# Performance work log

Measured on AMD Instinct MI355X. Metric: run time of the kernel, lower is better.

Reference implementation:

```python
import jax, jax.numpy as jnp
import numpy as np

B, N, C_IN = 8, 16384, 64
NPOINTS = 1024     # S: number of sampled centers (FPS)
NNEI = 32          # K: neighbors per center (ball query cap)
RADIUS = 0.2
EPS = 1e-5


def fps(pos, S):
    """Farthest point sampling, deterministic start at index 0. pos: [B,N,3] -> [B,S] int32."""
    b, n, _ = pos.shape

    def step(carry, _):
        dist, far = carry
        centroid = jnp.take_along_axis(pos, far[:, None, None], axis=1)  # [B,1,3]
        d = jnp.sum((pos - centroid) ** 2, axis=-1)                       # [B,N]
        dist = jnp.minimum(dist, d)
        return (dist, jnp.argmax(dist, axis=-1).astype(jnp.int32)), far

    init = (jnp.full((b, n), 1e10, pos.dtype), jnp.zeros((b,), jnp.int32))
    _, cent = jax.lax.scan(step, init, None, length=S)  # [S,B]
    return cent.T                                        # [B,S]


def gather(points, idx):
    """points [B,N,C], idx [B,...] -> [B,...,C] (per-batch fancy gather)."""
    return jax.vmap(lambda p, i: p[i])(points, idx)


def ball_query(pos, centers, radius, k):
    """Fixed-radius neighbor search. pos [B,N,3], centers [B,S,3] -> idx [B,S,K] int32.
    Pads short neighborhoods with the first in-radius point (the center itself)."""
    n = pos.shape[1]
    sqr = jnp.sum((centers[:, :, None, :] - pos[:, None, :, :]) ** 2, axis=-1)  # [B,S,N]
    idx = jnp.where(sqr <= radius * radius, jnp.arange(n, dtype=jnp.int32), n)
    idx = jnp.sort(idx, axis=-1)[..., :k]                                        # [B,S,K]
    first = idx[..., :1]
    return jnp.where(idx == n, first, idx)


def conv_bn_relu(x, w, b, g, be):
    """1x1 Conv2d + BatchNorm2d(training stats) + ReLU over grouped tensor x [B,S,K,Cin]."""
    h = jnp.einsum('bskc,cd->bskd', x, w) + b
    mu = jnp.mean(h, axis=(0, 1, 2), keepdims=True)
    var = jnp.mean((h - mu) ** 2, axis=(0, 1, 2), keepdims=True)
    h = (h - mu) * jax.lax.rsqrt(var + EPS) * g + be
    return jax.nn.relu(h)


def reference(pos, feat,
              w_sem1, b_sem1, g_sem1, be_sem1, w_sem2, b_sem2, g_sem2, be_sem2,
              w_geo1, b_geo1, g_geo1, be_geo1, w_geo2, b_geo2, g_geo2, be_geo2):
    centroids = fps(pos, NPOINTS)                       # [B,S]
    centers = gather(pos, centroids)                    # [B,S,3]
    idx = ball_query(pos, centers, RADIUS, NNEI)        # [B,S,K]

    grouped_pos = gather(pos, idx)                      # [B,S,K,3]
    grouped_feat = gather(feat, idx)                    # [B,S,K,C]
    center_rep = jnp.broadcast_to(centers[:, :, None, :], grouped_pos.shape)
    geo_in = jnp.concatenate([center_rep, grouped_pos], axis=-1)  # [B,S,K,6]

    h = conv_bn_relu(grouped_feat, w_sem1, b_sem1, g_sem1, be_sem1)
    h = conv_bn_relu(h, w_sem2, b_sem2, g_sem2, be_sem2)
    h_sem = jnp.max(h, axis=2)                          # [B,S,Cout] max-pool over neighbors

    hg = conv_bn_relu(geo_in, w_geo1, b_geo1, g_geo1, be_geo1)
    hg = conv_bn_relu(hg, w_geo2, b_geo2, g_geo2, be_geo2)
    h_geo = jnp.max(hg, axis=2)                         # [B,S,Cout]

    # original concatenates semantic and geo node features along dim 0
    return jnp.concatenate([h_sem, h_geo], axis=0)      # [2B,S,Cout]


def setup_inputs() -> dict:
    key = jax.random.key(0)
    ks = jax.random.split(key, 12)
    d = {
        'pos': jax.random.uniform(ks[0], (B, N, 3), jnp.float32),
        'feat': jax.random.normal(ks[1], (B, N, C_IN), jnp.float32),
        'w_sem1': jax.random.normal(ks[2], (64, 64), jnp.float32) * 0.05,
        'b_sem1': jnp.zeros((64,), jnp.float32),
        'g_sem1': jnp.ones((64,), jnp.float32),
        'be_sem1': jnp.zeros((64,), jnp.float32),
        'w_sem2': jax.random.normal(ks[3], (64, 128), jnp.float32) * 0.05,
        'b_sem2': jnp.zeros((128,), jnp.float32),
        'g_sem2': jnp.ones((128,), jnp.float32),
        'be_sem2': jnp.zeros((128,), jnp.float32),
        'w_geo1': jax.random.normal(ks[4], (6, 64), jnp.float32) * 0.05,
        'b_geo1': jnp.zeros((64,), jnp.float32),
        'g_geo1': jnp.ones((64,), jnp.float32),
        'be_geo1': jnp.zeros((64,), jnp.float32),
        'w_geo2': jax.random.normal(ks[5], (64, 128), jnp.float32) * 0.05,
        'b_geo2': jnp.zeros((128,), jnp.float32),
        'g_geo2': jnp.ones((128,), jnp.float32),
        'be_geo2': jnp.zeros((128,), jnp.float32),
    }
    return d
```

## Files before the change

kernel.cpp:

```cpp
#include <hip/hip_runtime.h>

#define NB 8
#define NPTS 16384
#define S 1024
#define KNEI 32
#define MROWS (NB*S*KNEI)

typedef float v2f __attribute__((ext_vector_type(2)));

#define DPP_MAXF0(CTRL, v) do {                                               \
    int _o = __builtin_amdgcn_update_dpp(0, __float_as_int(v),                \
                                         (CTRL), 0xF, 0xF, true);             \
    (v) = fmaxf((v), __int_as_float(_o));                                     \
  } while (0)

#define DPP_MINI(CTRL, v) do {                                                \
    int _o = __builtin_amdgcn_update_dpp((int)0x7fffffff, (v),                \
                                         (CTRL), 0xF, 0xF, false);            \
    (v) = (_o < (v)) ? _o : (v);                                              \
  } while (0)

#define DPP_MAXK0(CTRL, k) do {                                               \
    int _olo = __builtin_amdgcn_update_dpp(0, (int)(unsigned)(k),             \
                                           (CTRL), 0xF, 0xF, true);           \
    int _ohi = __builtin_amdgcn_update_dpp(0, (int)(unsigned)((k) >> 32),     \
                                           (CTRL), 0xF, 0xF, true);           \
    unsigned long long _ok = (((unsigned long long)(unsigned)_ohi) << 32)     \
                           | (unsigned)_olo;                                  \
    if (_ok > (k)) (k) = _ok;                                                 \
  } while (0)

#define DPP_ROW_SHR1   0x111
#define DPP_ROW_SHR2   0x112
#define DPP_ROW_SHR4   0x114
#define DPP_ROW_SHR8   0x118
#define DPP_ROW_BCAST15 0x142
#define DPP_ROW_BCAST31 0x143

__global__ __launch_bounds__(1024, 4) void fps_kernel(const float* __restrict__ pos,
                                                      float* __restrict__ centers,
                                                      float* __restrict__ sbuf){
#pragma clang fp contract(off)
  __shared__ int hist[4096];
  __shared__ int ts[1024];
  __shared__ unsigned short perm[16384];
  __shared__ unsigned long long lslotK[2][16];
  const int b = blockIdx.x;
  const int t = threadIdx.x;
  const int wid = t >> 6, lane = t & 63;
  const float* pb = pos + (size_t)b * NPTS * 3;
  float* ssx = sbuf + (size_t)b * 3 * NPTS;
  float* ssy = ssx + NPTS;
  float* ssz = ssy + NPTS;
  const int p0 = t * 16;

  float c[48];
  {
    const float4* src = (const float4*)(pb + (size_t)t*48);
#pragma unroll
    for (int q = 0; q < 12; ++q) *(float4*)&c[q*4] = src[q];
  }
  int cell[16];
#pragma unroll
  for (int j = 0; j < 16; ++j){
    float x = c[3*j], y = c[3*j+1], z = c[3*j+2];
    int ix = (int)(x * 16.f); ix = ix < 0 ? 0 : (ix > 15 ? 15 : ix);
    int iy = (int)(y * 16.f); iy = iy < 0 ? 0 : (iy > 15 ? 15 : iy);
    int iz = (int)(z * 16.f); iz = iz < 0 ? 0 : (iz > 15 ? 15 : iz);
    int m = 0;
#pragma unroll
    for (int k = 0; k < 4; ++k){
      m |= ((ix >> k) & 1) << (3*k + 2);
      m |= ((iy >> k) & 1) << (3*k + 1);
      m |= ((iz >> k) & 1) << (3*k + 0);
    }
    cell[j] = m;
  }
#pragma unroll
  for (int i = 0; i < 4; ++i) hist[t*4 + i] = 0;
  __syncthreads();
#pragma unroll
  for (int j = 0; j < 16; ++j) atomicAdd(&hist[cell[j]], 1);
  __syncthreads();
  int h0 = hist[t*4], h1 = hist[t*4+1], h2v = hist[t*4+2];
  ts[t] = h0 + h1 + h2v + hist[t*4+3];
  __syncthreads();
  for (int off = 1; off < 1024; off <<= 1){
    int add = (t >= off) ? ts[t - off] : 0;
    __syncthreads();
    ts[t] += add;
    __syncthreads();
  }
  {
    int base = (t == 0) ? 0 : ts[t-1];
    hist[t*4]   = base;
    hist[t*4+1] = base + h0;
    hist[t*4+2] = base + h0 + h1;
    hist[t*4+3] = base + h0 + h1 + h2v;
  }
  __syncthreads();
#pragma unroll
  for (int j = 0; j < 16; ++j){
    int dst = atomicAdd(&hist[cell[j]], 1);
    ssx[dst] = c[3*j];
    ssy[dst] = c[3*j+1];
    ssz[dst] = c[3*j+2];
    perm[dst] = (unsigned short)(p0 + j);
  }
  __syncthreads();

  v2f px[8], py[8], pz[8], dist[8];
  int perm_reg[8];
#pragma unroll
  for (int g = 0; g < 4; ++g){
    float4 vx = *(const float4*)&ssx[p0 + g*4];
    float4 vy = *(const float4*)&ssy[p0 + g*4];
    float4 vz = *(const float4*)&ssz[p0 + g*4];
    px[g*2]   = (v2f){vx.x, vx.y}; px[g*2+1] = (v2f){vx.z, vx.w};
    py[g*2]   = (v2f){vy.x, vy.y}; py[g*2+1] = (v2f){vy.z, vy.w};
    pz[g*2]   = (v2f){vz.x, vz.y}; pz[g*2+1] = (v2f){vz.z, vz.w};
  }
#pragma unroll
  for (int j = 0; j < 8; ++j){
    perm_reg[j] = (int)perm[p0 + 2*j] | ((int)perm[p0 + 2*j + 1] << 16);
  }
  float bxl = 1e30f, bxh = -1e30f, byl = 1e30f, byh = -1e30f;
  float bzl = 1e30f, bzh = -1e30f;
#pragma unroll
  for (int j = 0; j < 8; ++j){
    asm volatile("" : "+v"(px[j]), "+v"(py[j]), "+v"(pz[j]), "+v"(perm_reg[j]));
    bxl = fminf(bxl, fminf(px[j].x, px[j].y));
    bxh = fmaxf(bxh, fmaxf(px[j].x, px[j].y));
    byl = fminf(byl, fminf(py[j].x, py[j].y));
    byh = fmaxf(byh, fmaxf(py[j].x, py[j].y));
    bzl = fminf(bzl, fminf(pz[j].x, pz[j].y));
    bzh = fmaxf(bzh, fmaxf(pz[j].x, pz[j].y));
    dist[j] = (v2f){1e10f, 1e10f};
  }
  float ub = 1e10f;
  unsigned long long key = 0;
  float cx = pb[0], cy = pb[1], cz = pb[2];

  for (int s = 0; s < S; ++s){
    if (t == 0){
      float* cd = centers + (size_t)(b*S + s)*3;
      cd[0] = cx; cd[1] = cy; cd[2] = cz;
    }
    float lx = fmaxf(fmaxf(bxl - cx, cx - bxh), 0.f);
    float ly = fmaxf(fmaxf(byl - cy, cy - byh), 0.f);
    float lz = fmaxf(fmaxf(bzl - cz, cz - bzh), 0.f);
    float lb2 = ((lx*lx + ly*ly) + lz*lz);
    bool act = !(lb2 * 0.99999f >= ub);
    unsigned long long am = __ballot((int)act);
    if (am){
      if (act){
        v2f cx2 = (v2f){cx, cx}, cy2 = (v2f){cy, cy}, cz2 = (v2f){cz, cz};
        float nb = 0.0f;
#pragma unroll
        for (int j = 0; j < 8; ++j){
          v2f dx = px[j] - cx2;
          v2f dy = py[j] - cy2;
          v2f dz = pz[j] - cz2;
          v2f t1 = dx * dx;
          v2f t2 = dy * dy;
          v2f t3 = dz * dz;
          v2f d  = (t1 + t2) + t3;
          v2f od = dist[j];
          v2f nd = (v2f){__builtin_fminf(od.x, d.x), __builtin_fminf(od.y, d.y)};
          dist[j] = nd;
          nb = fmaxf(fmaxf(nb, nd.x), nd.y);
        }
        ub = nb;
      }
      float bv = ub;
      DPP_MAXF0(DPP_ROW_SHR1,   bv);
      DPP_MAXF0(DPP_ROW_SHR2,   bv);
      DPP_MAXF0(DPP_ROW_SHR4,   bv);
      DPP_MAXF0(DPP_ROW_SHR8,   bv);
      DPP_MAXF0(DPP_ROW_BCAST15, bv);
      DPP_MAXF0(DPP_ROW_BCAST31, bv);
      float bmw = __int_as_float(
          __builtin_amdgcn_readlane(__float_as_int(bv), 63));
      int mi = 0x7fffffff;
      if (ub == bmw){
#pragma unroll
        for (int j = 0; j < 8; ++j){
          if (dist[j].x == bmw){ int o = perm_reg[j] & 0xffff;         mi = o < mi ? o : mi; }
          if (dist[j].y == bmw){ int o = (perm_reg[j] >> 16) & 0xffff; mi = o < mi ? o : mi; }
        }
      }
      DPP_MINI(DPP_ROW_SHR1,   mi);
      DPP_MINI(DPP_ROW_SHR2,   mi);
      DPP_MINI(DPP_ROW_SHR4,   mi);
      DPP_MINI(DPP_ROW_SHR8,   mi);
      DPP_MINI(DPP_ROW_BCAST15, mi);
      DPP_MINI(DPP_ROW_BCAST31, mi);
      int miw = __builtin_amdgcn_readlane(mi, 63);
      key = ((unsigned long long)__float_as_uint(bmw) << 15)
          | (unsigned long long)(16384 - miw);
    }
    const int par = s & 1;
    if (lane == 0) lslotK[par][wid] = key;
    __syncthreads();
    unsigned long long kk = lslotK[par][lane & 15];
    int ufi_l = 16384 - (int)(kk & 0x7FFFull);
    const float* cpl = pb + (size_t)ufi_l*3;
    float wx = cpl[0], wy = cpl[1], wz = cpl[2];
    unsigned long long kko = kk;
    DPP_MAXK0(DPP_ROW_SHR1, kk);
    DPP_MAXK0(DPP_ROW_SHR2, kk);
    DPP_MAXK0(DPP_ROW_SHR4, kk);
    DPP_MAXK0(DPP_ROW_SHR8, kk);
    unsigned blo = (unsigned)__builtin_amdgcn_readlane((int)(unsigned)kk, 15);
    unsigned bhi = (unsigned)__builtin_amdgcn_readlane((int)(unsigned)(kk >> 32), 15);
    unsigned long long bkmax = (((unsigned long long)bhi) << 32) | blo;
    unsigned m16 = (unsigned)__ballot((int)(kko == bkmax)) & 0xffffu;
    int sidx = (int)__builtin_ctz(m16);
    cx = __int_as_float(__builtin_amdgcn_readlane(__float_as_int(wx), sidx));
    cy = __int_as_float(__builtin_amdgcn_readlane(__float_as_int(wy), sidx));
    cz = __int_as_float(__builtin_amdgcn_readlane(__float_as_int(wz), sidx));
  }
}

__global__ __launch_bounds__(256) void ballq_kernel(const float* __restrict__ pos,
                                                    const float* __restrict__ centers,
                                                    int* __restrict__ idx,
                                                    float* __restrict__ stats){
#pragma clang fp contract(off)
  if (blockIdx.x < 3) stats[blockIdx.x*256 + threadIdx.x] = 0.f;
  const float R2 = (float)(0.2*0.2);
  int wid  = blockIdx.x*4 + (threadIdx.x >> 6);
  int lane = threadIdx.x & 63;
  int b = wid >> 10;
  const float* pb = pos + (size_t)b * NPTS * 3;
  float cx = centers[wid*3+0], cy = centers[wid*3+1], cz = centers[wid*3+2];
  int* out = idx + wid*KNEI;
  int count = 0; int first = -1;
  for (int base = 0; base < NPTS; base += 64){
    int p = base + lane;
    float dx = pb[p*3+0]-cx, dy = pb[p*3+1]-cy, dz = pb[p*3+2]-cz;
    float t1 = dx*dx, t2 = dy*dy, t3 = dz*dz;
    float d = (t1 + t2) + t3;
    bool inr = d <= R2;
    unsigned long long mask = __ballot(inr);
    if (count == 0 && mask) first = base + __builtin_ctzll(mask);
    if (inr){
      int slot = count + __popcll(mask & ((1ull << lane) - 1ull));
      if (slot < KNEI) out[slot] = p;
    }
    count += __popcll(mask);
    if (count >= KNEI) break;
  }
  if (count < KNEI){
    for (int slot = count + lane; slot < KNEI; slot += 64) out[slot] = first;
  }
}

__global__ __launch_bounds__(256) void gemm1_both(const float* __restrict__ feat,
    const float* __restrict__ pos, const float* __restrict__ centers,
    const int* __restrict__ idx,
    const float* __restrict__ w_s, const float* __restrict__ b_s,
    float* __restrict__ h1s, float* __restrict__ st_s,
    const float* __restrict__ w_g, const float* __restrict__ b_g,
    float* __restrict__ h1g, float* __restrict__ st_g){
  __shared__ float smem[8448];
  const int tid = threadIdx.x;
  if (blockIdx.x < (MROWS/64)){
    float (*xst)[66] = (float(*)[66])smem;
    float (*wsh)[64] = (float(*)[64])(smem + 4224);
    const int m0 = blockIdx.x * 64;
#pragma unroll
    for (int i = 0; i < 4; ++i){
      int q = tid + i*256;
      int r = q >> 4, c4 = q & 15;
      *(float4*)&wsh[r][c4*4] = *(const float4*)&w_s[r*64 + c4*4];
    }
#pragma unroll
    for (int i = 0; i < 4; ++i){
      int q = tid + i*256;
      int r = q >> 4, c4 = q & 15;
      int m = m0 + r;
      int nb = idx[m];
      int b = m >> 15;
      const float* fr = feat + ((size_t)b*NPTS + nb)*64;
      float4 v = *(const float4*)&fr[c4*4];
      xst[c4*4+0][r] = v.x;
      xst[c4*4+1][r] = v.y;
      xst[c4*4+2][r] = v.z;
      xst[c4*4+3][r] = v.w;
    }
    __syncthreads();
    const int g  = tid & 7;
    const int rt = tid >> 3;
    const int r0 = rt * 2;
    float acc[2][8];
#pragma unroll
    for (int c = 0; c < 8; ++c){ float bb = b_s[g*8+c]; acc[0][c] = bb; acc[1][c] = bb; }
    for (int k = 0; k < 64; ++k){
      float x0 = xst[k][r0], x1 = xst[k][r0+1];
      float4 wa = *(float4*)&wsh[k][g*8];
      float4 wb = *(float4*)&wsh[k][g*8+4];
      float wv[8] = {wa.x,wa.y,wa.z,wa.w,wb.x,wb.y,wb.z,wb.w};
#pragma unroll
      for (int c = 0; c < 8; ++c){ acc[0][c] += x0*wv[c]; acc[1][c] += x1*wv[c]; }
    }
#pragma unroll
    for (int r = 0; r < 2; ++r){
      float* dst = h1s + (size_t)(m0 + r0 + r)*64 + g*8;
      *(float4*)dst     = make_float4(acc[r][0],acc[r][1],acc[r][2],acc[r][3]);
      *(float4*)(dst+4) = make_float4(acc[r][4],acc[r][5],acc[r][6],acc[r][7]);
    }
    float ls[8], lq[8];
#pragma unroll
    for (int c = 0; c < 8; ++c){
      ls[c] = acc[0][c] + acc[1][c];
      lq[c] = acc[0][c]*acc[0][c] + acc[1][c]*acc[1][c];
    }
    __syncthreads();
    float* red  = smem;
    float* redq = smem + 4224;
#pragma unroll
    for (int c = 0; c < 8; ++c){
      red[(g*8+c)*32 + rt]  = ls[c];
      redq[(g*8+c)*32 + rt] = lq[c];
    }
    __syncthreads();
    if (tid < 128){
      int c = tid & 63;
      const float* src = (tid < 64) ? red : redq;
      float a2 = 0.f;
      for (int i = 0; i < 32; ++i) a2 += src[c*32+i];
      atomicAdd(&st_s[(tid < 64 ? 0 : 64) + c], a2);
    }
  } else {
    float (*xs)[8]   = (float(*)[8])smem;
    float (*wsh)[64] = (float(*)[64])(smem + 512);
    float* red  = smem + 896;
    float* redq = smem + 2944;
    const int m0 = (blockIdx.x - (MROWS/64)) * 64;
    for (int i = tid; i < 384; i += 256) wsh[i >> 6][i & 63] = w_g[i];
    if (tid < 64){
      int m = m0 + tid;
      int grp = m >> 5;
      int b = m >> 15;
      int nb = idx[m];
      const float* cp = centers + (size_t)grp*3;
      const float* pp = pos + ((size_t)b*NPTS + nb)*3;
      xs[tid][0]=cp[0]; xs[tid][1]=cp[1]; xs[tid][2]=cp[2];
      xs[tid][3]=pp[0]; xs[tid][4]=pp[1]; xs[tid][5]=pp[2];
    }
    __syncthreads();
    const int g  = tid & 7;
    const int rt = tid >> 3;
    const int r0 = rt * 2;
    float acc[2][8];
#pragma unroll
    for (int c = 0; c < 8; ++c){ float bb = b_g[g*8+c]; acc[0][c]=bb; acc[1][c]=bb; }
#pragma unroll
    for (int k = 0; k < 6; ++k){
      float x0 = xs[r0][k], x1 = xs[r0+1][k];
      float4 wa = *(float4*)&wsh[k][g*8];
      float4 wb = *(float4*)&wsh[k][g*8+4];
      float wv[8] = {wa.x,wa.y,wa.z,wa.w,wb.x,wb.y,wb.z,wb.w};
#pragma unroll
      for (int c = 0; c < 8; ++c){ acc[0][c] += x0*wv[c]; acc[1][c] += x1*wv[c]; }
    }
#pragma unroll
    for (int r = 0; r < 2; ++r){
      float* dst = h1g + (size_t)(m0 + r0 + r)*64 + g*8;
      *(float4*)dst     = make_float4(acc[r][0],acc[r][1],acc[r][2],acc[r][3]);
      *(float4*)(dst+4) = make_float4(acc[r][4],acc[r][5],acc[r][6],acc[r][7]);
    }
    float ls[8], lq[8];
#pragma unroll
    for (int c = 0; c < 8; ++c){
      ls[c] = acc[0][c] + acc[1][c];
      lq[c] = acc[0][c]*acc[0][c] + acc[1][c]*acc[1][c];
    }
#pragma unroll
    for (int c = 0; c < 8; ++c){
      red[(g*8+c)*32 + rt]  = ls[c];
      redq[(g*8+c)*32 + rt] = lq[c];
    }
    __syncthreads();
    if (tid < 128){
      int c = tid & 63;
      const float* src = (tid < 64) ? red : redq;
      float a2 = 0.f;
      for (int i = 0; i < 32; ++i) a2 += src[c*32+i];
      atomicAdd(&st_g[(tid < 64 ? 0 : 64) + c], a2);
    }
  }
}

__global__ __launch_bounds__(256) void gemm2_both(
    const float* __restrict__ h1s, const float* __restrict__ st1,
    const float* __restrict__ g1,  const float* __restrict__ be1,
    const float* __restrict__ w_s2, const float* __restrict__ b_s2,
    float* __restrict__ hmax1, float* __restrict__ st2,
    const float* __restrict__ h1g, const float* __restrict__ st3,
    const float* __restrict__ g3,  const float* __restrict__ be3,
    const float* __restrict__ w_g2, const float* __restrict__ b_g2,
    float* __restrict__ hmax2, float* __restrict__ st4){
  __shared__ float smem[12416];
  __shared__ float abuf[64], dbuf[64];
  const int tid = threadIdx.x;
  const bool sem = blockIdx.x < (MROWS/64);
  const int bx = sem ? blockIdx.x : blockIdx.x - (MROWS/64);
  const float* hin  = sem ? h1s  : h1g;
  const float* w    = sem ? w_s2 : w_g2;
  const float* bias = sem ? b_s2 : b_g2;
  float* hmax       = sem ? hmax1 : hmax2;
  float* stat       = sem ? st2  : st4;
  float (*xst)[66]  = (float(*)[66])smem;
  float (*wsh)[128] = (float(*)[128])(smem + 4224);
  const int m0 = bx * 64;
  if (tid < 64){
    const float* st  = sem ? st1 : st3;
    const float* gam = sem ? g1  : g3;
    const float* bet = sem ? be1 : be3;
    const float invM = 1.0f / (float)MROWS;
    float mu  = st[tid] * invM;
    float ex2 = st[64 + tid] * invM;
    float var = ex2 - mu*mu;
    float aa = gam[tid] * rsqrtf(var + 1e-5f);
    abuf[tid] = aa;
    dbuf[tid] = bet[tid] - mu*aa;
  }
  __syncthreads();
#pragma unroll
  for (int i = 0; i < 8; ++i){
    int q = tid + i*256;
    int r = q >> 5, c4 = q & 31;
    *(float4*)&wsh[r][c4*4] = *(const float4*)&w[r*128 + c4*4];
  }
#pragma unroll
  for (int i = 0; i < 4; ++i){
    int q = tid + i*256;
    int r = q >> 4, c4 = q & 15;
    float4 v = *(const float4*)&hin[(size_t)(m0+r)*64 + c4*4];
    float a0 = abuf[c4*4+0], aA = abuf[c4*4+1], aB = abuf[c4*4+2], aC = abuf[c4*4+3];
    float d0 = dbuf[c4*4+0], dA = dbuf[c4*4+1], dB = dbuf[c4*4+2], dC = dbuf[c4*4+3];
    v.x = fmaxf(v.x*a0 + d0, 0.f);
    v.y = fmaxf(v.y*aA + dA, 0.f);
    v.z = fmaxf(v.z*aB + dB, 0.f);
    v.w = fmaxf(v.w*aC + dC, 0.f);
    xst[c4*4+0][r] = v.x;
    xst[c4*4+1][r] = v.y;
    xst[c4*4+2][r] = v.z;
    xst[c4*4+3][r] = v.w;
  }
  __syncthreads();
  const int g  = tid & 15;
  const int rt = tid >> 4;
  const int r0 = rt * 4;
  float acc[4][8];
#pragma unroll
  for (int c = 0; c < 8; ++c){
    float bb = bias[g*8+c];
    acc[0][c]=bb; acc[1][c]=bb; acc[2][c]=bb; acc[3][c]=bb;
  }
  for (int k = 0; k < 64; ++k){
    float x0 = xst[k][r0], x1 = xst[k][r0+1], x2 = xst[k][r0+2], x3 = xst[k][r0+3];
    float4 wa = *(float4*)&wsh[k][g*8];
    float4 wb = *(float4*)&wsh[k][g*8+4];
    float wv[8] = {wa.x,wa.y,wa.z,wa.w,wb.x,wb.y,wb.z,wb.w};
#pragma unroll
    for (int c = 0; c < 8; ++c){
      acc[0][c] += x0*wv[c]; acc[1][c] += x1*wv[c];
      acc[2][c] += x2*wv[c]; acc[3][c] += x3*wv[c];
    }
  }
  float ls[8], lq[8], tmax[8];
#pragma unroll
  for (int c = 0; c < 8; ++c){
    ls[c] = acc[0][c]+acc[1][c]+acc[2][c]+acc[3][c];
    lq[c] = acc[0][c]*acc[0][c]+acc[1][c]*acc[1][c]+acc[2][c]*acc[2][c]+acc[3][c]*acc[3][c];
    tmax[c] = fmaxf(fmaxf(acc[0][c],acc[1][c]), fmaxf(acc[2][c],acc[3][c]));
  }
  __syncthreads();
  float* red  = smem;
  float* mred = smem + 4224;
#pragma unroll
  for (int c = 0; c < 8; ++c){
    red[(g*8+c)*16 + rt]        = ls[c];
    red[2048 + (g*8+c)*16 + rt] = lq[c];
    mred[rt*128 + g*8 + c]      = tmax[c];
  }
  __syncthreads();
  {
    int c = tid & 127;
    int isq = tid >> 7;
    float a2 = 0.f;
    for (int i = 0; i < 16; ++i) a2 += red[isq*2048 + c*16 + i];
    atomicAdd(&stat[isq*128 + c], a2);
  }
  {
    int og = tid >> 7;
    int c  = tid & 127;
    float m = -3.4e38f;
#pragma unroll
    for (int i = 0; i < 8; ++i) m = fmaxf(m, mred[(og*8 + i)*128 + c]);
    hmax[(size_t)(bx*2 + og)*128 + c] = m;
  }
}

__global__ __launch_bounds__(256) void bnapply_both(const float* __restrict__ hmax1,
    const float* __restrict__ st2, const float* __restrict__ g2,
    const float* __restrict__ be2,
    const float* __restrict__ hmax2,
    const float* __restrict__ st4, const float* __restrict__ g4,
    const float* __restrict__ be4,
    float* __restrict__ out){
  const int half = NB*S*128;
  int i = blockIdx.x*256 + threadIdx.x;
  bool semh = i < half;
  int j = semh ? i : i - half;
  int c = j & 127;
  const float* st  = semh ? st2 : st4;
  const float* gam = semh ? g2  : g4;
  const float* bet = semh ? be2 : be4;
  const float invM = 1.0f / (float)MROWS;
  float mu  = st[c] * invM;
  float ex2 = st[128 + c] * invM;
  float var = ex2 - mu*mu;
  float aa = gam[c] * rsqrtf(var + 1e-5f);
  float dd = bet[c] - mu*aa;
  float hv = semh ? hmax1[j] : hmax2[j];
  out[i] = fmaxf(hv*aa + dd, 0.f);
}

extern "C" void kernel_launch(void* const* d_in, const int* in_sizes, int n_in,
                              void* d_out, int out_size, void* d_ws, size_t ws_size,
                              hipStream_t stream){
  const float* pos   = (const float*)d_in[0];
  const float* feat  = (const float*)d_in[1];
  const float* w_s1  = (const float*)d_in[2];
  const float* b_s1  = (const float*)d_in[3];
  const float* g_s1  = (const float*)d_in[4];
  const float* be_s1 = (const float*)d_in[5];
  const float* w_s2  = (const float*)d_in[6];
  const float* b_s2  = (const float*)d_in[7];
  const float* g_s2  = (const float*)d_in[8];
  const float* be_s2 = (const float*)d_in[9];
  const float* w_g1  = (const float*)d_in[10];
  const float* b_g1  = (const float*)d_in[11];
  const float* g_g1  = (const float*)d_in[12];
  const float* be_g1 = (const float*)d_in[13];
  const float* w_g2  = (const float*)d_in[14];
  const float* b_g2  = (const float*)d_in[15];
  const float* g_g2  = (const float*)d_in[16];
  const float* be_g2 = (const float*)d_in[17];
  float* outp = (float*)d_out;
  float* wsf  = (float*)d_ws;

  float* centers = wsf;
  int*   idxp    = (int*)(wsf + 24576);
  float* stats   = wsf + 24576 + 262144;
  float* h1s     = wsf + 288256;
  float* h1g     = h1s + (size_t)MROWS*64;
  float* sortbuf = h1g + (size_t)MROWS*64;
  float* hmax1   = sortbuf + 393216;
  float* hmax2   = hmax1 + 1048576;

  float* st1 = stats;
  float* st2 = stats + 128;
  float* st3 = stats + 384;
  float* st4 = stats + 512;

  fps_kernel<<<NB, 1024, 0, stream>>>(pos, centers, sortbuf);
  ballq_kernel<<<(NB*S)/4, 256, 0, stream>>>(pos, centers, idxp, stats);
  gemm1_both<<<2*(MROWS/64), 256, 0, stream>>>(feat, pos, centers, idxp,
      w_s1, b_s1, h1s, st1, w_g1, b_g1, h1g, st3);
  gemm2_both<<<2*(MROWS/64), 256, 0, stream>>>(
      h1s, st1, g_s1, be_s1, w_s2, b_s2, hmax1, st2,
      h1g, st3, g_g1, be_g1, w_g2, b_g2, hmax2, st4);
  bnapply_both<<<(2*NB*S*128)/256, 256, 0, stream>>>(
      hmax1, st2, g_s2, be_s2, hmax2, st4, g_g2, be_g2, outp);
}
```

Measured before the change: 1.668 ms.

## Replace FPS cross-wave argmax reduction with tagged shared atomicMax; swizzle gemm1 blocks

The per-iteration cross-wave argmax in FPS no longer goes through a double-buffered LDS slot array, a DPP 64-bit max and readlanes. Each wave now does one 64-bit atomicMax into a single shared cell, with an iteration tag in the high bits so the cell needs no reset. After one barrier every thread reads the winning key and loads the center coordinates from global memory. This shortens the serial critical path of the 1024-step loop, at the cost of LDS atomic contention and a dependent global load each step. The gemm1 block index is also remapped so consecutive blocks interleave across batches, which changes the gather locality.

```diff
diff --git a/kernel.cpp b/kernel.cpp
--- a/kernel.cpp
+++ b/kernel.cpp
@@ -18,16 +18,6 @@
     int _o = __builtin_amdgcn_update_dpp((int)0x7fffffff, (v),                \
                                          (CTRL), 0xF, 0xF, false);            \
     (v) = (_o < (v)) ? _o : (v);                                              \
-  } while (0)
-
-#define DPP_MAXK0(CTRL, k) do {                                               \
-    int _olo = __builtin_amdgcn_update_dpp(0, (int)(unsigned)(k),             \
-                                           (CTRL), 0xF, 0xF, true);           \
-    int _ohi = __builtin_amdgcn_update_dpp(0, (int)(unsigned)((k) >> 32),     \
-                                           (CTRL), 0xF, 0xF, true);           \
-    unsigned long long _ok = (((unsigned long long)(unsigned)_ohi) << 32)     \
-                           | (unsigned)_olo;                                  \
-    if (_ok > (k)) (k) = _ok;                                                 \
   } while (0)
 
 #define DPP_ROW_SHR1   0x111
@@ -44,10 +34,10 @@
   __shared__ int hist[4096];
   __shared__ int ts[1024];
   __shared__ unsigned short perm[16384];
-  __shared__ unsigned long long lslotK[2][16];
+  __shared__ unsigned long long wincell;
   const int b = blockIdx.x;
   const int t = threadIdx.x;
-  const int wid = t >> 6, lane = t & 63;
+  const int lane = t & 63;
   const float* pb = pos + (size_t)b * NPTS * 3;
   float* ssx = sbuf + (size_t)b * 3 * NPTS;
   float* ssy = ssx + NPTS;
@@ -107,6 +97,7 @@
     ssz[dst] = c[3*j+2];
     perm[dst] = (unsigned short)(p0 + j);
   }
+  if (t == 0) wincell = 0ull;
   __syncthreads();
 
   v2f px[8], py[8], pz[8], dist[8];
@@ -146,6 +137,7 @@
       float* cd = centers + (size_t)(b*S + s)*3;
       cd[0] = cx; cd[1] = cy; cd[2] = cz;
     }
+    const unsigned long long tag = (unsigned long long)(s + 1) << 47;
     float lx = fmaxf(fmaxf(bxl - cx, cx - bxh), 0.f);
     float ly = fmaxf(fmaxf(byl - cy, cy - byh), 0.f);
     float lz = fmaxf(fmaxf(bzl - cz, cz - bzh), 0.f);
@@ -199,26 +191,12 @@
       key = ((unsigned long long)__float_as_uint(bmw) << 15)
           | (unsigned long long)(16384 - miw);
     }
-    const int par = s & 1;
-    if (lane == 0) lslotK[par][wid] = key;
-    __syncthreads();
-    unsigned long long kk = lslotK[par][lane & 15];
-    int ufi_l = 16384 - (int)(kk & 0x7FFFull);
-    const float* cpl = pb + (size_t)ufi_l*3;
-    float wx = cpl[0], wy = cpl[1], wz = cpl[2];
-    unsigned long long kko = kk;
-    DPP_MAXK0(DPP_ROW_SHR1, kk);
-    DPP_MAXK0(DPP_ROW_SHR2, kk);
-    DPP_MAXK0(DPP_ROW_SHR4, kk);
-    DPP_MAXK0(DPP_ROW_SHR8, kk);
-    unsigned blo = (unsigned)__builtin_amdgcn_readlane((int)(unsigned)kk, 15);
-    unsigned bhi = (unsigned)__builtin_amdgcn_readlane((int)(unsigned)(kk >> 32), 15);
-    unsigned long long bkmax = (((unsigned long long)bhi) << 32) | blo;
-    unsigned m16 = (unsigned)__ballot((int)(kko == bkmax)) & 0xffffu;
-    int sidx = (int)__builtin_ctz(m16);
-    cx = __int_as_float(__builtin_amdgcn_readlane(__float_as_int(wx), sidx));
-    cy = __int_as_float(__builtin_amdgcn_readlane(__float_as_int(wy), sidx));
-    cz = __int_as_float(__builtin_amdgcn_readlane(__float_as_int(wz), sidx));
+    if (lane == 63) atomicMax(&wincell, tag | key);
+    __syncthreads();
+    unsigned long long wk = wincell;
+    int ufi = 16384 - (int)(wk & 0x7FFFull);
+    const float* cp = pb + (size_t)ufi*3;
+    cx = cp[0]; cy = cp[1]; cz = cp[2];
   }
 }
 
@@ -268,7 +246,8 @@
   if (blockIdx.x < (MROWS/64)){
     float (*xst)[66] = (float(*)[66])smem;
     float (*wsh)[64] = (float(*)[64])(smem + 4224);
-    const int m0 = blockIdx.x * 64;
+    const int sbx = ((blockIdx.x & 7) << 9) | (blockIdx.x >> 3);
+    const int m0 = sbx * 64;
 #pragma unroll
     for (int i = 0; i < 4; ++i){
       int q = tid + i*256;
```

Result: faster. 1.618 ms (-3.0%).
